# Kernel optimization log

Hardware: AMD Instinct MI355X
Metric: run time of the kernel (lower is better)

## Reference

```python
import jax, jax.numpy as jnp
import numpy as np

N_NODES = 100000
N_EDGES = 6_400_000
IN_DIM = 128


def gcn_conv(x, W, b, row, col, ew):
    """PyG GCNConv(normalize=True, add_self_loops=True) forward."""
    n = x.shape[0]
    loop = jnp.arange(n)
    row_sl = jnp.concatenate([row, loop])
    col_sl = jnp.concatenate([col, loop])
    ew_sl = jnp.concatenate([ew, jnp.ones((n,), ew.dtype)])
    # symmetric normalization: deg^{-1/2}[src] * w * deg^{-1/2}[dst]
    deg = jax.ops.segment_sum(ew_sl, col_sl, num_segments=n)
    safe_deg = jnp.where(deg > 0, deg, 1.0)
    dis = jnp.where(deg > 0, jax.lax.rsqrt(safe_deg), 0.0)
    norm = dis[row_sl] * ew_sl * dis[col_sl]
    h = x @ W  # [n, out_dim] linear transform first (small out_dim)
    # gather source features, scale, scatter-add into targets
    out = jax.ops.segment_sum(norm[:, None] * h[row_sl], col_sl, num_segments=n)
    return out + b


def setup_inputs() -> dict:
    key = jax.random.key(0)
    ks = jax.random.split(key, 12)
    X = jax.random.normal(ks[0], (N_NODES, IN_DIM), dtype=jnp.float32)
    edge_index = jax.random.randint(ks[1], (2, N_EDGES), 0, N_NODES, dtype=jnp.int64)
    edge_weight = jax.random.uniform(ks[2], (N_EDGES,), dtype=jnp.float32)

    def glorot(k, fan_in, fan_out):
        lim = np.sqrt(6.0 / (fan_in + fan_out)).astype(np.float32)
        return jax.random.uniform(k, (fan_in, fan_out), minval=-lim, maxval=lim, dtype=jnp.float32)

    return {
        "X": X,
        "edge_index": edge_index,
        "edge_weight": edge_weight,
        "W1": glorot(ks[3], IN_DIM, 12), "b1": jnp.zeros((12,), jnp.float32),
        "W2": glorot(ks[4], 12, 6), "b2": jnp.zeros((6,), jnp.float32),
        "W3": glorot(ks[5], 6, 3), "b3": jnp.zeros((3,), jnp.float32),
        "Wl": glorot(ks[6], 3, 1), "bl": jnp.zeros((1,), jnp.float32),
    }


def reference(X, edge_index, edge_weight, W1, b1, W2, b2, W3, b3, Wl, bl):
    row, col = edge_index[0], edge_index[1]
    h = jax.nn.relu(gcn_conv(X, W1, b1, row, col, edge_weight))
    # dropout p=0.2 is identity in eval mode
    h = jax.nn.relu(gcn_conv(h, W2, b2, row, col, edge_weight))
    h = jax.nn.relu(gcn_conv(h, W3, b3, row, col, edge_weight))
    out = jax.nn.sigmoid(h @ Wl + bl)
    return out.squeeze(1)  # [N]
```

## Files before the change

### kernel.cpp

```cpp
#include <hip/hip_runtime.h>
#include <cstdint>
#include <cstddef>

#define RANGE    128
#define RSHIFT   7
#define MAXBUCK  800
#define CSHIFT   12
#define CRANGE   4096
#define MAXC     32
#define FPB      32
#define CH_CNT   8192
#define CH_SC    4096
#define EPT      16
#define PAD      16
#define WSTR     132
#define STAGE_CAP 9216
#define KMAX     18
#define SCAP     3072

typedef _Float16 h8 __attribute__((ext_vector_type(8)));

#define GLOAD_LDS16(gsrc, ldsb)                                                   \
    __builtin_amdgcn_global_load_lds(                                             \
        (const __attribute__((address_space(1))) uint32_t*)(gsrc),                \
        (__attribute__((address_space(3))) uint32_t*)(ldsb), 16, 0, 0)

__global__ void zero_pad_kernel(int* __restrict__ p, int n) {
    int i = blockIdx.x * blockDim.x + threadIdx.x;
    if (i < n) p[i * PAD] = 0;
}

__global__ void count_kernel(const int* __restrict__ col, int* __restrict__ fcnt,
                             int nfine, int E) {
    __shared__ int lcnt[MAXBUCK];
    int tid = threadIdx.x;
    for (int i = tid; i < nfine; i += blockDim.x) lcnt[i] = 0;
    __syncthreads();
    int base = blockIdx.x * CH_CNT;
    int end  = min(E, base + CH_CNT);
    for (int e = base + tid; e < end; e += blockDim.x)
        atomicAdd(&lcnt[col[e] >> RSHIFT], 1);
    __syncthreads();
    for (int i = tid; i < nfine; i += blockDim.x)
        if (lcnt[i]) atomicAdd(&fcnt[i * PAD], lcnt[i]);
}

__global__ void scan_kernel(const int* __restrict__ fcnt, int* __restrict__ fbase,
                            int* __restrict__ fcur, int* __restrict__ cbase,
                            int* __restrict__ ccur, int* __restrict__ row_ptr,
                            int nfine, int ncoarse, int N, int E) {
    __shared__ int lds[1024];
    int T = threadIdx.x;
    int s = (T < nfine) ? fcnt[T * PAD] : 0;
    lds[T] = s;
    __syncthreads();
    for (int off = 1; off < 1024; off <<= 1) {
        int v = (T >= off) ? lds[T - off] : 0;
        __syncthreads();
        lds[T] += v;
        __syncthreads();
    }
    int excl = lds[T] - s;
    if (T < nfine) { fbase[T] = excl; fcur[T * PAD] = excl; }
    if ((T & (FPB - 1)) == 0 && (T >> 5) < ncoarse) {
        cbase[T >> 5] = excl;
        ccur[(T >> 5) * PAD] = excl;
    }
    if (T == 0) { fbase[nfine] = E; cbase[ncoarse] = E; row_ptr[N] = E; }
}

__global__ void coarse_scatter_kernel(const int* __restrict__ row, const int* __restrict__ col,
                                      const float* __restrict__ ew, int* __restrict__ ccur,
                                      uint2* __restrict__ partA, int ncoarse, int E) {
    __shared__ uint2 stage[CH_SC];
    __shared__ unsigned char sb[CH_SC];
    __shared__ int lcnt[MAXC], lofs[MAXC], gofs[MAXC];
    __shared__ int total_s;
    int tid = threadIdx.x;
    if (tid < MAXC) lcnt[tid] = 0;
    __syncthreads();
    int base = blockIdx.x * CH_SC;
    int cnt  = min(E - base, CH_SC);

    uint2 rec[EPT]; int rnk[EPT]; int bb[EPT];
#pragma unroll
    for (int k = 0; k < EPT; k++) {
        int idx = tid + (k << 8);
        if (idx < cnt) {
            int e = base + idx;
            int c = col[e];
            int b = c >> CSHIFT;
            bb[k]  = b;
            rec[k] = make_uint2((unsigned)row[e] | ((unsigned)(c & (CRANGE - 1)) << 17),
                                __float_as_uint(ew[e]));
            rnk[k] = atomicAdd(&lcnt[b], 1);
        }
    }
    __syncthreads();
    if (tid == 0) {
        int run = 0;
        for (int i = 0; i < ncoarse; i++) { lofs[i] = run; run += lcnt[i]; }
        total_s = run;
    }
    __syncthreads();
    if (tid < ncoarse) {
        int c = lcnt[tid];
        if (c) {
            int g = atomicAdd(&ccur[tid * PAD], c);
            gofs[tid] = g - lofs[tid];
        }
    }
#pragma unroll
    for (int k = 0; k < EPT; k++) {
        int idx = tid + (k << 8);
        if (idx < cnt) {
            int p = lofs[bb[k]] + rnk[k];
            stage[p] = rec[k];
            sb[p] = (unsigned char)bb[k];
        }
    }
    __syncthreads();
    int total = total_s;
    for (int i = tid; i < total; i += 256)
        partA[gofs[sb[i]] + i] = stage[i];
}

__global__ __launch_bounds__(256, 3)
void fine_scatter_kernel(const uint2* __restrict__ partA, const int* __restrict__ cbase,
                                    int* __restrict__ fcur, uint2* __restrict__ partB,
                                    int nfine, int ncoarse, int E) {
    __shared__ uint2 stage[CH_SC];
    __shared__ unsigned short sb[CH_SC];
    __shared__ int lcnt[MAXBUCK], lofs[MAXBUCK], gofs[MAXBUCK];
    __shared__ int tmp[256];
    __shared__ int scb[MAXC + 1];
    __shared__ int rlo_s, total_s;
    int tid = threadIdx.x;
    int base = blockIdx.x * CH_SC;
    int cnt  = min(E - base, CH_SC);
    if (tid <= ncoarse) scb[tid] = cbase[tid];
    for (int i = tid; i < nfine; i += 256) lcnt[i] = 0;
    if (tid == 0) {
        int r = 0;
        while (r < ncoarse - 1 && cbase[r + 1] <= base) ++r;
        rlo_s = r;
    }
    __syncthreads();
    int rlo = rlo_s;

    uint2 rec[EPT]; int rnk[EPT]; int ff[EPT];
#pragma unroll
    for (int k = 0; k < EPT; k++) {
        int idx = tid + (k << 8);
        if (idx < cnt) {
            int e = base + idx;
            uint2 v = partA[e];
            int r = rlo;
            while (e >= scb[r + 1]) ++r;
            int col12 = (int)((v.x >> 17) & (CRANGE - 1));
            int f = (r << 5) | (col12 >> RSHIFT);
            ff[k]  = f;
            rec[k] = make_uint2((v.x & 0x1FFFFu) | ((unsigned)(col12 & (RANGE - 1)) << 17), v.y);
            rnk[k] = atomicAdd(&lcnt[f], 1);
        }
    }
    __syncthreads();
    {
        const int Cc = (nfine + 255) >> 8;
        int b0 = tid * Cc;
        int s = 0;
        for (int i = 0; i < Cc; i++) {
            int idx = b0 + i;
            if (idx < nfine) s += lcnt[idx];
        }
        tmp[tid] = s;
        __syncthreads();
        for (int off = 1; off < 256; off <<= 1) {
            int v = (tid >= off) ? tmp[tid - off] : 0;
            __syncthreads();
            tmp[tid] += v;
            __syncthreads();
        }
        int run = tmp[tid] - s;
        for (int i = 0; i < Cc; i++) {
            int idx = b0 + i;
            if (idx < nfine) { lofs[idx] = run; run += lcnt[idx]; }
        }
        if (tid == 255) total_s = tmp[255];
    }
    __syncthreads();
    for (int i = tid; i < nfine; i += 256) {
        int c = lcnt[i];
        if (c) {
            int g = atomicAdd(&fcur[i * PAD], c);
            gofs[i] = g - lofs[i];
        }
    }
#pragma unroll
    for (int k = 0; k < EPT; k++) {
        int idx = tid + (k << 8);
        if (idx < cnt) {
            int p = lofs[ff[k]] + rnk[k];
            stage[p] = rec[k];
            sb[p] = (unsigned short)ff[k];
        }
    }
    __syncthreads();
    int total = total_s;
    for (int i = tid; i < total; i += 256)
        partB[gofs[sb[i]] + i] = stage[i];
}

__global__ __launch_bounds__(512, 4)
void bucket_csr_kernel(const uint2* __restrict__ part, const int* __restrict__ bbase,
                       int* __restrict__ row_ptr, float* __restrict__ dis,
                       uint2* __restrict__ csr, int N) {
    extern __shared__ uint2 stage[];
    __shared__ int   scnt[RANGE];
    __shared__ int   sscan[RANGE];
    __shared__ float sdeg[RANGE];
    __shared__ float sdis[RANGE];
    int b = blockIdx.x, tid = threadIdx.x;
    int s = bbase[b], t = bbase[b + 1];
    int cnt = t - s;
    int lim = min(cnt, STAGE_CAP);
    if (tid < RANGE) { scnt[tid] = 0; sdeg[tid] = 1.0f; }
    {
        int wave = tid >> 6, lane = tid & 63;
        int iters = (lim + 1023) >> 10;
        for (int it = 0; it < iters; ++it) {
            int recBase = (it << 10) + (wave << 7);
            const uint2* src = part + s + recBase + (lane << 1);
            GLOAD_LDS16(src, (char*)stage + ((size_t)recBase << 3));
        }
    }
    asm volatile("s_waitcnt vmcnt(0)" ::: "memory");
    __syncthreads();
    for (int idx = tid; idx < lim; idx += 512) {
        uint2 r = stage[idx];
        int c = (r.x >> 17) & (RANGE - 1);
        atomicAdd(&scnt[c], 1);
        atomicAdd(&sdeg[c], __uint_as_float(r.y));
    }
    for (int idx = STAGE_CAP + tid; idx < cnt; idx += 512) {
        uint2 r = part[s + idx];
        int c = (r.x >> 17) & (RANGE - 1);
        atomicAdd(&scnt[c], 1);
        atomicAdd(&sdeg[c], __uint_as_float(r.y));
    }
    __syncthreads();
    int cnt_t = 0;
    if (tid < RANGE) { cnt_t = scnt[tid]; sscan[tid] = cnt_t; }
    __syncthreads();
    for (int off = 1; off < RANGE; off <<= 1) {
        int v = 0;
        if (tid < RANGE && tid >= off) v = sscan[tid - off];
        __syncthreads();
        if (tid < RANGE) sscan[tid] += v;
        __syncthreads();
    }
    if (tid < RANGE) {
        int excl = sscan[tid] - cnt_t;
        int node = b * RANGE + tid;
        float dn = rsqrtf(sdeg[tid]);
        sdis[tid] = dn;
        if (node < N) {
            row_ptr[node] = s + excl;
            dis[node] = dn;
        }
        scnt[tid] = excl;
    }
    __syncthreads();

    if (cnt <= STAGE_CAP) {
        uint2 rc[KMAX]; int rp[KMAX];
#pragma unroll
        for (int k = 0; k < KMAX; k++) {
            int idx = tid + k * 512;
            if (idx < cnt) {
                uint2 r = stage[idx];
                int c   = (r.x >> 17) & (RANGE - 1);
                float v = sdis[c] * __uint_as_float(r.y);
                rp[k] = atomicAdd(&scnt[c], 1);
                rc[k] = make_uint2(r.x & 0x1FFFFu, __float_as_uint(v));
            }
        }
        __syncthreads();
#pragma unroll
        for (int k = 0; k < KMAX; k++) {
            int idx = tid + k * 512;
            if (idx < cnt) stage[rp[k]] = rc[k];
        }
        __syncthreads();
        for (int i = tid; i < cnt; i += 512)
            csr[s + i] = stage[i];
    } else {
        for (int idx = tid; idx < cnt; idx += 512) {
            uint2 r = (idx < STAGE_CAP) ? stage[idx] : part[s + idx];
            int c   = (r.x >> 17) & (RANGE - 1);
            float v = sdis[c] * __uint_as_float(r.y);
            int off = atomicAdd(&scnt[c], 1);
            csr[s + off] = make_uint2(r.x & 0x1FFFFu, __float_as_uint(v));
        }
    }
}

__global__ void lin1_kernel(const float* __restrict__ X, const float* __restrict__ W1,
                            const float* __restrict__ dis, uint4* __restrict__ t1, int n) {
    __shared__ float w1t[12 * WSTR];
    int tid = threadIdx.x;
    for (int i = tid; i < 128 * 12; i += 256) {
        int k = i / 12, o = i - k * 12;
        w1t[o * WSTR + k] = W1[i];
    }
    __syncthreads();
    int gt   = blockIdx.x * 256 + tid;
    int node = gt >> 3;
    int sub  = gt & 7;
    if (node >= n) return;

    const float4* xp = (const float4*)(X + (size_t)node * 128 + sub * 16);
    float4 x0 = xp[0], x1 = xp[1], x2 = xp[2], x3 = xp[3];

    float res[12];
#pragma unroll
    for (int o = 0; o < 12; o++) {
        const float4* wp = (const float4*)(w1t + o * WSTR + sub * 16);
        float4 w0 = wp[0], w1v = wp[1], w2 = wp[2], w3 = wp[3];
        float s;
        s  = x0.x * w0.x + x0.y * w0.y + x0.z * w0.z + x0.w * w0.w;
        s += x1.x * w1v.x + x1.y * w1v.y + x1.z * w1v.z + x1.w * w1v.w;
        s += x2.x * w2.x + x2.y * w2.y + x2.z * w2.z + x2.w * w2.w;
        s += x3.x * w3.x + x3.y * w3.y + x3.z * w3.z + x3.w * w3.w;
        res[o] = s;
    }
#pragma unroll
    for (int o = 0; o < 12; o++) {
        res[o] += __shfl_xor(res[o], 1, 64);
        res[o] += __shfl_xor(res[o], 2, 64);
        res[o] += __shfl_xor(res[o], 4, 64);
    }
    if (sub == 0) {
        h8 a, b;
#pragma unroll
        for (int o = 0; o < 8; o++) a[o] = (_Float16)res[o];
#pragma unroll
        for (int o = 0; o < 4; o++) b[o] = (_Float16)res[8 + o];
#pragma unroll
        for (int o = 4; o < 8; o++) b[o] = (_Float16)0.f;
        uint4 ua = __builtin_bit_cast(uint4, a);
        uint4 ub = __builtin_bit_cast(uint4, b);
        ub.z = __float_as_uint(dis[node]);
        ub.w = 0u;
        uint4* dst = t1 + (size_t)node * 2;
        dst[0] = ua;
        dst[1] = ub;
    }
}

template <int DIN, int ROWW, int DOUT, bool LAST>
__global__ __launch_bounds__(256)
void agg_kernel(const int* __restrict__ row_ptr, const uint2* __restrict__ csr,
                const uint4* __restrict__ hin,
                const float* __restrict__ b_this, const float* __restrict__ W_next,
                const float* __restrict__ b_next, void* __restrict__ hout_v, int n) {
    __shared__ uint2 scsr[SCAP];
    int tid = threadIdx.x;
    int nodeBase = blockIdx.x << 5;
    int node = nodeBase + (tid >> 3);
    int sub  = tid & 7;
    int endNode  = min(nodeBase + 32, n);
    int blkStart = row_ptr[nodeBase];
    int blkEnd   = row_ptr[endNode];
    int blkCnt   = blkEnd - blkStart;
    int lim = min(blkCnt, SCAP);
    {
        int wave = tid >> 6, lane = tid & 63;
        int iters = (lim + 511) >> 9;
        for (int it = 0; it < iters; ++it) {
            int recBase = (it << 9) + (wave << 7);
            const uint2* src = csr + blkStart + recBase + (lane << 1);
            GLOAD_LDS16(src, (char*)scsr + ((size_t)recBase << 3));
        }
    }
    asm volatile("s_waitcnt vmcnt(0)" ::: "memory");
    __syncthreads();

    if (node >= n) return;
    int start = row_ptr[node];
    int end   = row_ptr[node + 1];
    float acc[DIN], acc2[DIN];
#pragma unroll
    for (int d = 0; d < DIN; d++) { acc[d] = 0.f; acc2[d] = 0.f; }

    auto body = [&](uint2 r, float* a_) {
        int src    = (int)(r.x);
        float ewdd = __uint_as_float(r.y);
        const uint4* hr = hin + (size_t)src * ROWW;
        if constexpr (DIN == 12) {
            uint4 ua = hr[0], ub = hr[1];
            float norm = ewdd * __uint_as_float(ub.z);
            h8 a = __builtin_bit_cast(h8, ua);
            h8 b = __builtin_bit_cast(h8, ub);
#pragma unroll
            for (int d = 0; d < 8; d++) a_[d] += norm * (float)a[d];
#pragma unroll
            for (int d = 0; d < 4; d++) a_[8 + d] += norm * (float)b[d];
        } else if constexpr (DIN == 6) {
            uint4 u = hr[0];
            float norm = ewdd * __uint_as_float(u.w);
            h8 a = __builtin_bit_cast(h8, u);
#pragma unroll
            for (int d = 0; d < 6; d++) a_[d] += norm * (float)a[d];
        } else {
            uint4 u = hr[0];
            float norm = ewdd * __uint_as_float(u.z);
            h8 a = __builtin_bit_cast(h8, u);
#pragma unroll
            for (int d = 0; d < 3; d++) a_[d] += norm * (float)a[d];
        }
    };

    if (blkCnt <= SCAP) {
        int ls = start - blkStart;
        int le = end - blkStart;
        int e = ls + sub;
        for (; e + 8 < le; e += 16) {
            uint2 r0 = scsr[e];
            uint2 r1 = scsr[e + 8];
            body(r0, acc);
            body(r1, acc2);
        }
        if (e < le) body(scsr[e], acc);
    } else {
        int e = start + sub;
        for (; e + 8 < end; e += 16) {
            uint2 r0 = csr[e];
            uint2 r1 = csr[e + 8];
            body(r0, acc);
            body(r1, acc2);
        }
        if (e < end) body(csr[e], acc);
    }

#pragma unroll
    for (int d = 0; d < DIN; d++) {
        acc[d] += acc2[d];
        acc[d] += __shfl_xor(acc[d], 1, 64);
        acc[d] += __shfl_xor(acc[d], 2, 64);
        acc[d] += __shfl_xor(acc[d], 4, 64);
    }

    if (sub == 0) {
        const uint4* hn = hin + (size_t)node * ROWW;
        float v[DIN];
        float dn;
        if constexpr (DIN == 12) {
            uint4 ua = hn[0], ub = hn[1];
            dn = __uint_as_float(ub.z);
            float s2 = dn * dn;
            h8 a = __builtin_bit_cast(h8, ua);
            h8 b = __builtin_bit_cast(h8, ub);
#pragma unroll
            for (int d = 0; d < 8; d++) v[d] = fmaxf(acc[d] + s2 * (float)a[d] + b_this[d], 0.f);
#pragma unroll
            for (int d = 0; d < 4; d++) v[8 + d] = fmaxf(acc[8 + d] + s2 * (float)b[d] + b_this[8 + d], 0.f);
        } else if constexpr (DIN == 6) {
            uint4 u = hn[0];
            dn = __uint_as_float(u.w);
            float s2 = dn * dn;
            h8 a = __builtin_bit_cast(h8, u);
#pragma unroll
            for (int d = 0; d < 6; d++) v[d] = fmaxf(acc[d] + s2 * (float)a[d] + b_this[d], 0.f);
        } else {
            uint4 u = hn[0];
            dn = __uint_as_float(u.z);
            float s2 = dn * dn;
            h8 a = __builtin_bit_cast(h8, u);
#pragma unroll
            for (int d = 0; d < 3; d++) v[d] = fmaxf(acc[d] + s2 * (float)a[d] + b_this[d], 0.f);
        }
        if constexpr (!LAST) {
            float o[DOUT];
#pragma unroll
            for (int oo = 0; oo < DOUT; oo++) {
                float z = 0.f;
#pragma unroll
                for (int d = 0; d < DIN; d++) z += v[d] * W_next[d * DOUT + oo];
                o[oo] = z;
            }
            h8 w;
#pragma unroll
            for (int oo = 0; oo < 8; oo++) w[oo] = (_Float16)0.f;
#pragma unroll
            for (int oo = 0; oo < DOUT; oo++) w[oo] = (_Float16)o[oo];
            uint4 uw = __builtin_bit_cast(uint4, w);
            if constexpr (DOUT == 6) uw.w = __float_as_uint(dn);
            else                     uw.z = __float_as_uint(dn);
            ((uint4*)hout_v)[node] = uw;
        } else {
            float z = b_next[0];
#pragma unroll
            for (int d = 0; d < DIN; d++) z += v[d] * W_next[d];
            ((float*)hout_v)[node] = 1.0f / (1.0f + expf(-z));
        }
    }
}

extern "C" void kernel_launch(void* const* d_in, const int* in_sizes, int n_in,
                              void* d_out, int out_size, void* d_ws, size_t ws_size,
                              hipStream_t stream) {
    const float* X  = (const float*)d_in[0];
    const int*   ei = (const int*)d_in[1];
    const float* ew = (const float*)d_in[2];
    const float* W1 = (const float*)d_in[3];
    const float* b1 = (const float*)d_in[4];
    const float* W2 = (const float*)d_in[5];
    const float* b2 = (const float*)d_in[6];
    const float* W3 = (const float*)d_in[7];
    const float* b3 = (const float*)d_in[8];
    const float* Wl = (const float*)d_in[9];
    const float* bl = (const float*)d_in[10];
    float* out = (float*)d_out;

    const int N = in_sizes[0] / 128;
    const int E = in_sizes[1] / 2;
    const int* row = ei;
    const int* col = ei + E;
    const int nfine   = (N + RANGE - 1) >> RSHIFT;
    const int ncoarse = (N + CRANGE - 1) >> CSHIFT;

    char* ws = (char*)d_ws;
    size_t off = 0;
    auto carve = [&](size_t bytes) -> void* {
        void* p = ws + off;
        off += (bytes + 255) & ~(size_t)255;
        return p;
    };
    int*   fcnt    = (int*)  carve((size_t)MAXBUCK * PAD * 4);
    int*   fcur    = (int*)  carve((size_t)MAXBUCK * PAD * 4);
    int*   ccur    = (int*)  carve((size_t)MAXC * PAD * 4);
    int*   cbase   = (int*)  carve((size_t)(MAXC + 1) * 4);
    int*   fbase   = (int*)  carve((size_t)(MAXBUCK + 1) * 4);
    int*   row_ptr = (int*)  carve((size_t)(N + 1) * 4);
    float* dis     = (float*)carve((size_t)N * 4);
    uint2* partA   = (uint2*)carve((size_t)E * 8);
    uint2* partB   = (uint2*)carve((size_t)(E + 1024) * 8);
    uint2* csr = partA;
    uint4* t1  = (uint4*)partB;
    uint4* t2  = t1 + (size_t)N * 2;
    uint4* t3  = t2 + (size_t)N;
    (void)ws_size; (void)n_in; (void)out_size;

    const int bCnt = (E + CH_CNT - 1) / CH_CNT;
    const int bSc  = (E + CH_SC - 1) / CH_SC;
    const int bL   = ((size_t)N * 8 + 255) / 256;
    const int bA   = (N + 31) / 32;

    zero_pad_kernel<<<(nfine + 255) / 256, 256, 0, stream>>>(fcnt, nfine);
    count_kernel<<<bCnt, 256, 0, stream>>>(col, fcnt, nfine, E);
    scan_kernel<<<1, 1024, 0, stream>>>(fcnt, fbase, fcur, cbase, ccur, row_ptr,
                                        nfine, ncoarse, N, E);
    coarse_scatter_kernel<<<bSc, 256, 0, stream>>>(row, col, ew, ccur, partA, ncoarse, E);
    fine_scatter_kernel<<<bSc, 256, 0, stream>>>(partA, cbase, fcur, partB, nfine, ncoarse, E);
    bucket_csr_kernel<<<nfine, 512, (size_t)STAGE_CAP * sizeof(uint2), stream>>>(
        partB, fbase, row_ptr, dis, csr, N);
    lin1_kernel<<<bL, 256, 0, stream>>>(X, W1, dis, t1, N);
    agg_kernel<12, 2, 6, false><<<bA, 256, 0, stream>>>(row_ptr, csr, t1, b1, W2, nullptr, t2, N);
    agg_kernel< 6, 1, 3, false><<<bA, 256, 0, stream>>>(row_ptr, csr, t2, b2, W3, nullptr, t3, N);
    agg_kernel< 3, 1, 1, true ><<<bA, 256, 0, stream>>>(row_ptr, csr, t3, b3, Wl, bl, out, N);
}
```

Before: 466.5 us.

## Pack CSR records into 32-bit words with fp16 edge weight

```diff
diff --git a/kernel.cpp b/kernel.cpp
--- a/kernel.cpp
+++ b/kernel.cpp
@@ -15,7 +15,6 @@
 #define PAD      16
 #define WSTR     132
 #define STAGE_CAP 9216
-#define KMAX     18
 #define SCAP     3072
 
 typedef _Float16 h8 __attribute__((ext_vector_type(8)));
@@ -24,6 +23,15 @@
     __builtin_amdgcn_global_load_lds(                                             \
         (const __attribute__((address_space(1))) uint32_t*)(gsrc),                \
         (__attribute__((address_space(3))) uint32_t*)(ldsb), 16, 0, 0)
+
+static __device__ __forceinline__ unsigned pack_rec(int src, float w) {
+    unsigned short hb = __builtin_bit_cast(unsigned short, (_Float16)w);
+    return (unsigned)src | ((unsigned)hb << 17);
+}
+static __device__ __forceinline__ float rec_w(unsigned rec) {
+    unsigned short hb = (unsigned short)(rec >> 17);
+    return (float)__builtin_bit_cast(_Float16, hb);
+}
 
 __global__ void zero_pad_kernel(int* __restrict__ p, int n) {
     int i = blockIdx.x * blockDim.x + threadIdx.x;
@@ -211,11 +219,11 @@
         partB[gofs[sb[i]] + i] = stage[i];
 }
 
-__global__ __launch_bounds__(512, 4)
+__global__ __launch_bounds__(512, 8)
 void bucket_csr_kernel(const uint2* __restrict__ part, const int* __restrict__ bbase,
                        int* __restrict__ row_ptr, float* __restrict__ dis,
-                       uint2* __restrict__ csr, int N) {
-    extern __shared__ uint2 stage[];
+                       unsigned* __restrict__ csr, int N) {
+    __shared__ unsigned cst[STAGE_CAP];
     __shared__ int   scnt[RANGE];
     __shared__ int   sscan[RANGE];
     __shared__ float sdeg[RANGE];
@@ -223,27 +231,10 @@
     int b = blockIdx.x, tid = threadIdx.x;
     int s = bbase[b], t = bbase[b + 1];
     int cnt = t - s;
-    int lim = min(cnt, STAGE_CAP);
     if (tid < RANGE) { scnt[tid] = 0; sdeg[tid] = 1.0f; }
-    {
-        int wave = tid >> 6, lane = tid & 63;
-        int iters = (lim + 1023) >> 10;
-        for (int it = 0; it < iters; ++it) {
-            int recBase = (it << 10) + (wave << 7);
-            const uint2* src = part + s + recBase + (lane << 1);
-            GLOAD_LDS16(src, (char*)stage + ((size_t)recBase << 3));
-        }
-    }
-    asm volatile("s_waitcnt vmcnt(0)" ::: "memory");
-    __syncthreads();
-    for (int idx = tid; idx < lim; idx += 512) {
-        uint2 r = stage[idx];
-        int c = (r.x >> 17) & (RANGE - 1);
-        atomicAdd(&scnt[c], 1);
-        atomicAdd(&sdeg[c], __uint_as_float(r.y));
-    }
-    for (int idx = STAGE_CAP + tid; idx < cnt; idx += 512) {
-        uint2 r = part[s + idx];
+    __syncthreads();
+    for (int i = tid; i < cnt; i += 512) {
+        uint2 r = part[s + i];
         int c = (r.x >> 17) & (RANGE - 1);
         atomicAdd(&scnt[c], 1);
         atomicAdd(&sdeg[c], __uint_as_float(r.y));
@@ -271,38 +262,20 @@
         scnt[tid] = excl;
     }
     __syncthreads();
-
-    if (cnt <= STAGE_CAP) {
-        uint2 rc[KMAX]; int rp[KMAX];
-#pragma unroll
-        for (int k = 0; k < KMAX; k++) {
-            int idx = tid + k * 512;
-            if (idx < cnt) {
-                uint2 r = stage[idx];
-                int c   = (r.x >> 17) & (RANGE - 1);
-                float v = sdis[c] * __uint_as_float(r.y);
-                rp[k] = atomicAdd(&scnt[c], 1);
-                rc[k] = make_uint2(r.x & 0x1FFFFu, __float_as_uint(v));
-            }
-        }
-        __syncthreads();
-#pragma unroll
-        for (int k = 0; k < KMAX; k++) {
-            int idx = tid + k * 512;
-            if (idx < cnt) stage[rp[k]] = rc[k];
-        }
-        __syncthreads();
-        for (int i = tid; i < cnt; i += 512)
-            csr[s + i] = stage[i];
-    } else {
-        for (int idx = tid; idx < cnt; idx += 512) {
-            uint2 r = (idx < STAGE_CAP) ? stage[idx] : part[s + idx];
-            int c   = (r.x >> 17) & (RANGE - 1);
-            float v = sdis[c] * __uint_as_float(r.y);
-            int off = atomicAdd(&scnt[c], 1);
-            csr[s + off] = make_uint2(r.x & 0x1FFFFu, __float_as_uint(v));
-        }
-    }
+    for (int i = tid; i < cnt; i += 512) {
+        uint2 r = part[s + i];
+        int c   = (r.x >> 17) & (RANGE - 1);
+        int src = (int)(r.x & 0x1FFFFu);
+        float w = sdis[c] * __uint_as_float(r.y);
+        unsigned rec = pack_rec(src, w);
+        int p = atomicAdd(&scnt[c], 1);
+        if (p < STAGE_CAP) cst[p] = rec;
+        else               csr[s + p] = rec;
+    }
+    __syncthreads();
+    int lim = min(cnt, STAGE_CAP);
+    for (int i = tid; i < lim; i += 512)
+        csr[s + i] = cst[i];
 }
 
 __global__ void lin1_kernel(const float* __restrict__ X, const float* __restrict__ W1,
@@ -360,11 +333,11 @@
 
 template <int DIN, int ROWW, int DOUT, bool LAST>
 __global__ __launch_bounds__(256)
-void agg_kernel(const int* __restrict__ row_ptr, const uint2* __restrict__ csr,
+void agg_kernel(const int* __restrict__ row_ptr, const unsigned* __restrict__ csr,
                 const uint4* __restrict__ hin,
                 const float* __restrict__ b_this, const float* __restrict__ W_next,
                 const float* __restrict__ b_next, void* __restrict__ hout_v, int n) {
-    __shared__ uint2 scsr[SCAP];
+    __shared__ unsigned scsr[SCAP];
     int tid = threadIdx.x;
     int nodeBase = blockIdx.x << 5;
     int node = nodeBase + (tid >> 3);
@@ -376,11 +349,11 @@
     int lim = min(blkCnt, SCAP);
     {
         int wave = tid >> 6, lane = tid & 63;
-        int iters = (lim + 511) >> 9;
+        int iters = (lim + 1023) >> 10;
         for (int it = 0; it < iters; ++it) {
-            int recBase = (it << 9) + (wave << 7);
-            const uint2* src = csr + blkStart + recBase + (lane << 1);
-            GLOAD_LDS16(src, (char*)scsr + ((size_t)recBase << 3));
+            int recBase = (it << 10) + (wave << 8);
+            const unsigned* src = csr + blkStart + recBase + (lane << 2);
+            GLOAD_LDS16(src, (char*)scsr + ((size_t)recBase << 2));
         }
     }
     asm volatile("s_waitcnt vmcnt(0)" ::: "memory");
@@ -393,13 +366,13 @@
 #pragma unroll
     for (int d = 0; d < DIN; d++) { acc[d] = 0.f; acc2[d] = 0.f; }
 
-    auto body = [&](uint2 r, float* a_) {
-        int src    = (int)(r.x);
-        float ewdd = __uint_as_float(r.y);
+    auto body = [&](unsigned r, float* a_) {
+        int src  = (int)(r & 0x1FFFFu);
+        float wq = rec_w(r);
         const uint4* hr = hin + (size_t)src * ROWW;
         if constexpr (DIN == 12) {
             uint4 ua = hr[0], ub = hr[1];
-            float norm = ewdd * __uint_as_float(ub.z);
+            float norm = wq * __uint_as_float(ub.z);
             h8 a = __builtin_bit_cast(h8, ua);
             h8 b = __builtin_bit_cast(h8, ub);
 #pragma unroll
@@ -408,13 +381,13 @@
             for (int d = 0; d < 4; d++) a_[8 + d] += norm * (float)b[d];
         } else if constexpr (DIN == 6) {
             uint4 u = hr[0];
-            float norm = ewdd * __uint_as_float(u.w);
+            float norm = wq * __uint_as_float(u.w);
             h8 a = __builtin_bit_cast(h8, u);
 #pragma unroll
             for (int d = 0; d < 6; d++) a_[d] += norm * (float)a[d];
         } else {
             uint4 u = hr[0];
-            float norm = ewdd * __uint_as_float(u.z);
+            float norm = wq * __uint_as_float(u.z);
             h8 a = __builtin_bit_cast(h8, u);
 #pragma unroll
             for (int d = 0; d < 3; d++) a_[d] += norm * (float)a[d];
@@ -426,8 +399,8 @@
         int le = end - blkStart;
         int e = ls + sub;
         for (; e + 8 < le; e += 16) {
-            uint2 r0 = scsr[e];
-            uint2 r1 = scsr[e + 8];
+            unsigned r0 = scsr[e];
+            unsigned r1 = scsr[e + 8];
             body(r0, acc);
             body(r1, acc2);
         }
@@ -435,8 +408,8 @@
     } else {
         int e = start + sub;
         for (; e + 8 < end; e += 16) {
-            uint2 r0 = csr[e];
-            uint2 r1 = csr[e + 8];
+            unsigned r0 = csr[e];
+            unsigned r1 = csr[e + 8];
             body(r0, acc);
             body(r1, acc2);
         }
@@ -545,8 +518,8 @@
     int*   row_ptr = (int*)  carve((size_t)(N + 1) * 4);
     float* dis     = (float*)carve((size_t)N * 4);
     uint2* partA   = (uint2*)carve((size_t)E * 8);
-    uint2* partB   = (uint2*)carve((size_t)(E + 1024) * 8);
-    uint2* csr = partA;
+    uint2* partB   = (uint2*)carve((size_t)(E + STAGE_CAP) * 8);
+    unsigned* csr = (unsigned*)partA;
     uint4* t1  = (uint4*)partB;
     uint4* t2  = t1 + (size_t)N * 2;
     uint4* t3  = t2 + (size_t)N;
@@ -563,8 +536,7 @@
                                         nfine, ncoarse, N, E);
     coarse_scatter_kernel<<<bSc, 256, 0, stream>>>(row, col, ew, ccur, partA, ncoarse, E);
     fine_scatter_kernel<<<bSc, 256, 0, stream>>>(partA, cbase, fcur, partB, nfine, ncoarse, E);
-    bucket_csr_kernel<<<nfine, 512, (size_t)STAGE_CAP * sizeof(uint2), stream>>>(
-        partB, fbase, row_ptr, dis, csr, N);
+    bucket_csr_kernel<<<nfine, 512, 0, stream>>>(partB, fbase, row_ptr, dis, csr, N);
     lin1_kernel<<<bL, 256, 0, stream>>>(X, W1, dis, t1, N);
     agg_kernel<12, 2, 6, false><<<bA, 256, 0, stream>>>(row_ptr, csr, t1, b1, W2, nullptr, t2, N);
     agg_kernel< 6, 1, 3, false><<<bA, 256, 0, stream>>>(row_ptr, csr, t2, b2, W3, nullptr, t3, N);
```

After: 452.9 us. -2.9%, faster.
